# Optimization experiments

Measured on AMD Instinct MI355X. Metric: run time of the kernel, lower is better.

Reference implementation:

```python
import jax, jax.numpy as jnp
import numpy as np

D_MODEL = 512
D_AUX = 64
B, N = 8, 2048


def setup_inputs() -> dict:
    key = jax.random.key(0)
    ks = jax.random.split(key, 12)
    lim = 1.0 / np.sqrt(D_MODEL)  # torch Linear default init scale
    inp = {
        "x": jax.random.normal(ks[0], (B, N, D_MODEL), dtype=jnp.float32),
        "query_aux": jax.random.normal(ks[1], (B, N, D_AUX), dtype=jnp.float32),
        "key_aux": jax.random.normal(ks[2], (B, N, D_AUX), dtype=jnp.float32),
        "adjacency_mask": jax.random.randint(ks[3], (B, N, N), 0, 2, dtype=jnp.int32),
        "merge_coefficients": jnp.float32(0.3),
        "Wq": jax.random.uniform(ks[4], (D_MODEL, D_MODEL), jnp.float32, -lim, lim),
        "bq": jax.random.uniform(ks[5], (D_MODEL,), jnp.float32, -lim, lim),
        "Wk": jax.random.uniform(ks[6], (D_MODEL, D_MODEL), jnp.float32, -lim, lim),
        "bk": jax.random.uniform(ks[7], (D_MODEL,), jnp.float32, -lim, lim),
        "Wv": jax.random.uniform(ks[8], (D_MODEL, D_MODEL), jnp.float32, -lim, lim),
        "bv": jax.random.uniform(ks[9], (D_MODEL,), jnp.float32, -lim, lim),
        "threshold": jnp.float32(0.5),
    }
    return inp


def reference(x, query_aux, key_aux, adjacency_mask, merge_coefficients,
              Wq, bq, Wk, bk, Wv, bv, threshold):
    d_model = x.shape[-1]
    d_aux = key_aux.shape[-1]
    scale = jnp.asarray(d_model, x.dtype) ** 0.5
    scale_aux = jnp.asarray(d_aux, x.dtype) ** 0.5

    q = x @ Wq.T + bq  # [B,N,D]
    k = x @ Wk.T + bk
    v = x @ Wv.T + bv

    scores = jnp.einsum('bnd,bmd->bnm', q, k) / scale  # [B,N,N]
    scores_aux = jnp.einsum('bnd,bmd->bnm', query_aux, key_aux) / scale_aux

    # data-dependent merge: where aux score nonzero AND score above learned threshold
    merge_mask = (scores_aux != 0) & (scores > threshold)
    merged = (1.0 - merge_coefficients) * scores + merge_coefficients * scores_aux
    scores = jnp.where(merge_mask, merged, scores)

    mask_value = jnp.finfo(scores.dtype).min
    scores = jnp.where(adjacency_mask == 0, mask_value, scores)

    weights = jax.nn.softmax(scores, axis=-1)
    return jnp.einsum('bnm,bmd->bnd', weights, v)
```

## Files before the change

kernel.cpp:

```cpp
#include <hip/hip_runtime.h>
#include <cstdint>

#define SEQ    2048
#define DM     512
#define DAUX   64

typedef _Float16 f16;
typedef __attribute__((ext_vector_type(2))) _Float16 f16x2;
typedef __attribute__((ext_vector_type(4))) _Float16 f16x4;
typedef __attribute__((ext_vector_type(8))) _Float16 f16x8;
typedef __attribute__((ext_vector_type(4))) float fx4;
typedef __attribute__((ext_vector_type(16))) float fx16;

__device__ __forceinline__ void g2l16(const void* g, void* l) {
  __builtin_amdgcn_global_load_lds(
      (__attribute__((address_space(1))) void*)const_cast<void*>(g),
      (__attribute__((address_space(3))) void*)l, 16, 0, 0);
}

__device__ __forceinline__ void stage32(const f16* __restrict__ g0, int stride,
                                        f16* lds, int t) {
#pragma unroll
  for (int p = 0; p < 2; ++p) {
    int L = p * 256 + t;
    int row = L >> 2;
    int jp = L & 3;
    int jl = jp ^ ((row >> 1) & 3);
    g2l16(g0 + (size_t)row * stride + jl * 8, lds + L * 8);
  }
}
__device__ __forceinline__ f16x8 frag32(const f16* lds, int row, int kq) {
  int jp = (kq >> 3) ^ ((row >> 1) & 3);
  return *(const f16x8*)(lds + row * 32 + jp * 8);
}

__device__ __forceinline__ void stage64(const f16* __restrict__ g0, int stride,
                                        f16* lds, int t) {
#pragma unroll
  for (int p = 0; p < 4; ++p) {
    int L = p * 256 + t;
    int row = L >> 3;
    int jp = L & 7;
    int jl = jp ^ (row & 7);
    g2l16(g0 + (size_t)row * stride + jl * 8, lds + L * 8);
  }
}
__device__ __forceinline__ f16x8 frag64(const f16* lds, int row, int kq) {
  int jp = (kq >> 3) ^ (row & 7);
  return *(const f16x8*)(lds + row * 64 + jp * 8);
}

__device__ __forceinline__ void chunk3_32(const f16* Ah, const f16* Al,
                                          const f16* Bh, const f16* Bl,
                                          fx16 acc[2][2], int wm, int wn, int lane) {
  const int r31 = lane & 31;
  const int kq = (lane >> 5) * 8;
#pragma unroll
  for (int k0 = 0; k0 < 32; k0 += 16) {
    f16x8 ah[2], al[2];
#pragma unroll
    for (int it = 0; it < 2; ++it) {
      int row = wm * 64 + it * 32 + r31;
      ah[it] = frag32(Ah, row, k0 + kq);
      al[it] = frag32(Al, row, k0 + kq);
    }
#pragma unroll
    for (int jt = 0; jt < 2; ++jt) {
      int col = wn * 64 + jt * 32 + r31;
      f16x8 bh = frag32(Bh, col, k0 + kq);
      f16x8 bl = frag32(Bl, col, k0 + kq);
#pragma unroll
      for (int it = 0; it < 2; ++it) {
        acc[it][jt] = __builtin_amdgcn_mfma_f32_32x32x16_f16(ah[it], bh, acc[it][jt], 0, 0, 0);
        acc[it][jt] = __builtin_amdgcn_mfma_f32_32x32x16_f16(ah[it], bl, acc[it][jt], 0, 0, 0);
        acc[it][jt] = __builtin_amdgcn_mfma_f32_32x32x16_f16(al[it], bh, acc[it][jt], 0, 0, 0);
      }
    }
  }
}

__device__ __forceinline__ void chunk1_64(const f16* A, const f16* B,
                                          fx16 acc[2][2], int wm, int wn, int lane) {
  const int r31 = lane & 31;
  const int kq = (lane >> 5) * 8;
#pragma unroll
  for (int k0 = 0; k0 < 64; k0 += 16) {
    f16x8 a[2];
#pragma unroll
    for (int it = 0; it < 2; ++it)
      a[it] = frag64(A, wm * 64 + it * 32 + r31, k0 + kq);
#pragma unroll
    for (int jt = 0; jt < 2; ++jt) {
      f16x8 b = frag64(B, wn * 64 + jt * 32 + r31, k0 + kq);
#pragma unroll
      for (int it = 0; it < 2; ++it)
        acc[it][jt] = __builtin_amdgcn_mfma_f32_32x32x16_f16(a[it], b, acc[it][jt], 0, 0, 0);
    }
  }
}

__global__ __launch_bounds__(256) void convert_split(
    const float* __restrict__ x, const float* __restrict__ Wq,
    const float* __restrict__ Wk, const float* __restrict__ Wv,
    f16* __restrict__ xh, f16* __restrict__ xl,
    f16* __restrict__ Wh, f16* __restrict__ Wl) {
  int idx = blockIdx.x * 256 + threadIdx.x;
  const float* src; f16* dh; f16* dl; size_t off;
  if (idx < 2097152) { src = x; off = (size_t)idx; dh = xh; dl = xl; }
  else {
    int rr = idx - 2097152;
    int w = rr >> 16, o = rr & 65535;
    src = (w == 0) ? Wq : (w == 1) ? Wk : Wv;
    off = (size_t)o;
    dh = Wh + (size_t)w * 262144; dl = Wl + (size_t)w * 262144;
  }
  float4 v = ((const float4*)src)[off];
  float vv[4] = {v.x, v.y, v.z, v.w};
  f16x4 hv, lv;
#pragma unroll
  for (int i = 0; i < 4; ++i) {
    float s = vv[i] * 32.0f;
    f16 hi = (f16)s;
    hv[i] = hi;
    lv[i] = (f16)(s - (float)hi);
  }
  *(f16x4*)(dh + off * 4) = hv;
  *(f16x4*)(dl + off * 4) = lv;
}

__global__ __launch_bounds__(256) void qkv_mfma(
    const f16* __restrict__ xh, const f16* __restrict__ xl,
    const f16* __restrict__ Wh, const f16* __restrict__ Wl,
    const float* __restrict__ bq, const float* __restrict__ bk, const float* __restrict__ bv,
    f16* __restrict__ qh, f16* __restrict__ ql,
    f16* __restrict__ kh, f16* __restrict__ kl,
    f16* __restrict__ vt) {
  __shared__ __align__(16) f16 sm[32768];
  const int t = threadIdx.x;
  const int i0 = blockIdx.x * 128, j0 = blockIdx.y * 128, z = blockIdx.z;
  const f16* WhZ = Wh + (size_t)z * 262144;
  const f16* WlZ = Wl + (size_t)z * 262144;
  const int lane = t & 63, wave = t >> 6;
  const int wm = wave >> 1, wn = wave & 1;
  const int r31 = lane & 31, half = lane >> 5;
  fx16 acc[2][2] = {};
  const f16* xhB = xh + (size_t)i0 * DM;
  const f16* xlB = xl + (size_t)i0 * DM;
  const f16* WhB = WhZ + (size_t)j0 * DM;
  const f16* WlB = WlZ + (size_t)j0 * DM;
  if (z < 2) {
    stage32(xhB, DM, sm, t);
    stage32(xlB, DM, sm + 4096, t);
    stage32(WhB, DM, sm + 8192, t);
    stage32(WlB, DM, sm + 12288, t);
    __syncthreads();
    for (int c = 0; c < 16; ++c) {
      f16* cur = sm + (c & 1) * 16384;
      if (c < 15) {
        f16* nxt = sm + ((c + 1) & 1) * 16384;
        int d0 = (c + 1) * 32;
        stage32(xhB + d0, DM, nxt, t);
        stage32(xlB + d0, DM, nxt + 4096, t);
        stage32(WhB + d0, DM, nxt + 8192, t);
        stage32(WlB + d0, DM, nxt + 12288, t);
      }
      chunk3_32(cur, cur + 4096, cur + 8192, cur + 12288, acc, wm, wn, lane);
      if (c < 15) __syncthreads();
    }
  } else {
    stage64(xhB, DM, sm, t);
    stage64(WhB, DM, sm + 8192, t);
    __syncthreads();
    for (int c = 0; c < 8; ++c) {
      f16* cur = sm + (c & 1) * 16384;
      if (c < 7) {
        f16* nxt = sm + ((c + 1) & 1) * 16384;
        int d0 = (c + 1) * 64;
        stage64(xhB + d0, DM, nxt, t);
        stage64(WhB + d0, DM, nxt + 8192, t);
      }
      chunk1_64(cur, cur + 8192, acc, wm, wn, lane);
      if (c < 7) __syncthreads();
    }
  }
  const float* bias = (z == 0) ? bq : (z == 1) ? bk : bv;
  if (z < 2) {
    f16* oh = z ? kh : qh;  f16* ol = z ? kl : ql;
#pragma unroll
    for (int it = 0; it < 2; ++it)
#pragma unroll
      for (int jt = 0; jt < 2; ++jt) {
        int j = j0 + wn * 64 + jt * 32 + r31;
        float bj = bias[j];
#pragma unroll
        for (int r = 0; r < 16; ++r) {
          int ib = i0 + wm * 64 + it * 32 + (r & 3) + 8 * (r >> 2) + 4 * half;
          float val = acc[it][jt][r] * (1.0f / 1024.0f) + bj;
          float s = val * 32.0f;
          f16 hi = (f16)s;
          oh[(size_t)ib * DM + j] = hi;
          ol[(size_t)ib * DM + j] = (f16)(s - (float)hi);
        }
      }
  } else {
#pragma unroll
    for (int it = 0; it < 2; ++it)
#pragma unroll
      for (int jt = 0; jt < 2; ++jt) {
        int j = j0 + wn * 64 + jt * 32 + r31;
        float bj = bias[j];
#pragma unroll
        for (int q4 = 0; q4 < 4; ++q4) {
          int ib = i0 + wm * 64 + it * 32 + 8 * q4 + 4 * half;
          int bb = ib >> 11, nb = ib & 2047;
          f16x4 hv;
#pragma unroll
          for (int g = 0; g < 4; ++g)
            hv[g] = (f16)(acc[it][jt][q4 * 4 + g] * (1.0f / 1024.0f) + bj);
          *(f16x4*)(vt + ((size_t)(bb * DM + j)) * SEQ + nb) = hv;
        }
      }
  }
}

__global__ __launch_bounds__(256) void scores_mfma(
    const f16* __restrict__ qh, const f16* __restrict__ ql,
    const f16* __restrict__ kh, const f16* __restrict__ kl,
    const float* __restrict__ qa, const float* __restrict__ ka,
    const int* __restrict__ adj,
    const float* __restrict__ mc_p, const float* __restrict__ thr_p,
    f16* __restrict__ S16) {
  __shared__ __align__(16) f16 sm[32768];
  const int t = threadIdx.x;
  const int n0 = blockIdx.x * 128, m0 = blockIdx.y * 128, b = blockIdx.z;
  const int lane = t & 63, wave = t >> 6;
  const int wm = wave >> 1, wn = wave & 1;
  const int r31 = lane & 31, half = lane >> 5;
  const int kq = half * 8;

  const f16* qhB = qh + ((size_t)b * SEQ + n0) * DM;
  const f16* qlB = ql + ((size_t)b * SEQ + n0) * DM;
  const f16* khB = kh + ((size_t)b * SEQ + m0) * DM;
  const f16* klB = kl + ((size_t)b * SEQ + m0) * DM;

  stage32(qhB, DM, sm, t);
  stage32(qlB, DM, sm + 4096, t);
  stage32(khB, DM, sm + 8192, t);
  stage32(klB, DM, sm + 12288, t);

  f16* QAl = sm + 16384;
  f16* KAl = sm + 24576;
  const float* QAb = qa + ((size_t)b * SEQ + n0) * DAUX;
  const float* KAb = ka + ((size_t)b * SEQ + m0) * DAUX;
#pragma unroll
  for (int p = 0; p < 4; ++p) {
    int L8 = p * 256 + t;
    int row = L8 >> 3, jb = L8 & 7;
    int c8 = jb * 8;
    int jp = jb ^ (row & 7);
    float4 u0 = *(const float4*)(QAb + (size_t)row * DAUX + c8);
    float4 u1 = *(const float4*)(QAb + (size_t)row * DAUX + c8 + 4);
    f16x8 hq = {(f16)u0.x,(f16)u0.y,(f16)u0.z,(f16)u0.w,(f16)u1.x,(f16)u1.y,(f16)u1.z,(f16)u1.w};
    *(f16x8*)(QAl + row * 64 + jp * 8) = hq;
    float4 w0 = *(const float4*)(KAb + (size_t)row * DAUX + c8);
    float4 w1 = *(const float4*)(KAb + (size_t)row * DAUX + c8 + 4);
    f16x8 hk = {(f16)w0.x,(f16)w0.y,(f16)w0.z,(f16)w0.w,(f16)w1.x,(f16)w1.y,(f16)w1.z,(f16)w1.w};
    *(f16x8*)(KAl + row * 64 + jp * 8) = hk;
  }
  __syncthreads();

  f16x2 sax2[2][2][8];
  {
    fx16 aacc[2][2] = {};
#pragma unroll
    for (int k0 = 0; k0 < 64; k0 += 16) {
      f16x8 qaf[2];
#pragma unroll
      for (int it = 0; it < 2; ++it)
        qaf[it] = frag64(QAl, wm * 64 + it * 32 + r31, k0 + kq);
#pragma unroll
      for (int jt = 0; jt < 2; ++jt) {
        f16x8 kaf = frag64(KAl, wn * 64 + jt * 32 + r31, k0 + kq);
#pragma unroll
        for (int it = 0; it < 2; ++it)
          aacc[it][jt] = __builtin_amdgcn_mfma_f32_32x32x16_f16(qaf[it], kaf, aacc[it][jt], 0, 0, 0);
      }
    }
#pragma unroll
    for (int it = 0; it < 2; ++it)
#pragma unroll
      for (int jt = 0; jt < 2; ++jt)
#pragma unroll
        for (int r = 0; r < 16; ++r)
          sax2[it][jt][r >> 1][r & 1] = (f16)aacc[it][jt][r];
  }
  __syncthreads();

  fx16 acc[2][2] = {};
  for (int c = 0; c < 16; ++c) {
    f16* cur = sm + (c & 1) * 16384;
    if (c < 15) {
      f16* nxt = sm + ((c + 1) & 1) * 16384;
      int d0 = (c + 1) * 32;
      stage32(qhB + d0, DM, nxt, t);
      stage32(qlB + d0, DM, nxt + 4096, t);
      stage32(khB + d0, DM, nxt + 8192, t);
      stage32(klB + d0, DM, nxt + 12288, t);
    }
    chunk3_32(cur, cur + 4096, cur + 8192, cur + 12288, acc, wm, wn, lane);
    if (c < 15) __syncthreads();
  }

  const float mc = *mc_p, thr = *thr_p;
  const float invC = 1.0f / (1024.0f * 22.62741699796952f);
#pragma unroll
  for (int it = 0; it < 2; ++it)
#pragma unroll
    for (int jt = 0; jt < 2; ++jt) {
      int col = m0 + wn * 64 + jt * 32 + r31;
#pragma unroll
      for (int r = 0; r < 16; ++r) {
        int row = n0 + wm * 64 + it * 32 + (r & 3) + 8 * (r >> 2) + 4 * half;
        size_t rbase = ((size_t)b * SEQ + row) * SEQ;
        float s = acc[it][jt][r] * invC;
        float sa = (float)sax2[it][jt][r >> 1][r & 1] * 0.125f;
        if (sa != 0.0f && s > thr) s = (1.0f - mc) * s + mc * sa;
        if (adj[rbase + col] == 0) s = -65504.0f;
        S16[rbase + col] = (f16)s;
      }
    }
}

__global__ __launch_bounds__(256) void softmax_p(
    f16* __restrict__ S16, float* __restrict__ rowsum) {
  const int wv = threadIdx.x >> 6, ln = threadIdx.x & 63;
  const size_t row = (size_t)blockIdx.x * 4 + wv;
  f16* Sr = S16 + row * SEQ;
  f16x8 v[4];
  float vals[32];
#pragma unroll
  for (int j = 0; j < 4; ++j) {
    v[j] = *(const f16x8*)(Sr + j * 512 + ln * 8);
#pragma unroll
    for (int i = 0; i < 8; ++i) vals[j * 8 + i] = (float)v[j][i];
  }
  float m = vals[0];
#pragma unroll
  for (int i = 1; i < 32; ++i) m = fmaxf(m, vals[i]);
#pragma unroll
  for (int off = 1; off < 64; off <<= 1) m = fmaxf(m, __shfl_xor(m, off, 64));
  float z = 0.f;
  f16x8 p16[4];
#pragma unroll
  for (int j = 0; j < 4; ++j)
#pragma unroll
    for (int i = 0; i < 8; ++i) {
      f16 p = (f16)(__expf(vals[j * 8 + i] - m) * 1024.0f);
      p16[j][i] = p;
      z += (float)p;
    }
#pragma unroll
  for (int off = 1; off < 64; off <<= 1) z += __shfl_xor(z, off, 64);
  if (ln == 0) rowsum[row] = z;
#pragma unroll
  for (int j = 0; j < 4; ++j)
    *(f16x8*)(Sr + j * 512 + ln * 8) = p16[j];
}

__global__ __launch_bounds__(256) void pv_mfma(
    const f16* __restrict__ P16, const f16* __restrict__ vt,
    const float* __restrict__ rowsum, float* __restrict__ O) {
  __shared__ __align__(16) f16 sm[32768];
  const int t = threadIdx.x;
  const int n0 = blockIdx.x * 128, d0 = blockIdx.y * 128, b = blockIdx.z;
  const int lane = t & 63, wave = t >> 6;
  const int wm = wave >> 1, wn = wave & 1;
  const int r31 = lane & 31, half = lane >> 5;
  fx16 acc[2][2] = {};
  const f16* Pb = P16 + ((size_t)b * SEQ + n0) * SEQ;
  const f16* Vb = vt + ((size_t)b * DM + d0) * SEQ;
  stage64(Pb, SEQ, sm, t);
  stage64(Vb, SEQ, sm + 8192, t);
  __syncthreads();
  for (int c = 0; c < 32; ++c) {
    f16* cur = sm + (c & 1) * 16384;
    if (c < 31) {
      f16* nxt = sm + ((c + 1) & 1) * 16384;
      int m0 = (c + 1) * 64;
      stage64(Pb + m0, SEQ, nxt, t);
      stage64(Vb + m0, SEQ, nxt + 8192, t);
    }
    chunk1_64(cur, cur + 8192, acc, wm, wn, lane);
    if (c < 31) __syncthreads();
  }
#pragma unroll
  for (int it = 0; it < 2; ++it)
#pragma unroll
    for (int jt = 0; jt < 2; ++jt) {
      int d = d0 + wn * 64 + jt * 32 + r31;
#pragma unroll
      for (int r = 0; r < 16; ++r) {
        int n = n0 + wm * 64 + it * 32 + (r & 3) + 8 * (r >> 2) + 4 * half;
        float inv = 1.0f / rowsum[(size_t)b * SEQ + n];
        O[((size_t)b * SEQ + n) * DM + d] = acc[it][jt][r] * inv;
      }
    }
}

extern "C" void kernel_launch(void* const* d_in, const int* in_sizes, int n_in,
                              void* d_out, int out_size, void* d_ws, size_t ws_size,
                              hipStream_t stream) {
  const float* x   = (const float*)d_in[0];
  const float* qa  = (const float*)d_in[1];
  const float* ka  = (const float*)d_in[2];
  const int*   adj = (const int*)d_in[3];
  const float* mc  = (const float*)d_in[4];
  const float* Wq  = (const float*)d_in[5];
  const float* bq  = (const float*)d_in[6];
  const float* Wk  = (const float*)d_in[7];
  const float* bk  = (const float*)d_in[8];
  const float* Wv  = (const float*)d_in[9];
  const float* bv  = (const float*)d_in[10];
  const float* thr = (const float*)d_in[11];
  float* out = (float*)d_out;

  f16* qh  = (f16*)d_ws;
  f16* ql  = qh + 8388608;
  f16* kh  = ql + 8388608;
  f16* kl  = kh + 8388608;
  f16* vt  = kl + 8388608;
  f16* S16 = vt + 8388608;
  float* rowsum = (float*)(S16 + 33554432);
  f16* xh = S16;
  f16* xl = xh + 8388608;
  f16* Wh = xl + 8388608;
  f16* Wl = Wh + 786432;

  convert_split<<<8960, 256, 0, stream>>>(x, Wq, Wk, Wv, xh, xl, Wh, Wl);
  qkv_mfma<<<dim3(128, 4, 3), 256, 0, stream>>>(xh, xl, Wh, Wl, bq, bk, bv,
                                                qh, ql, kh, kl, vt);
  scores_mfma<<<dim3(16, 16, 8), 256, 0, stream>>>(qh, ql, kh, kl, qa, ka, adj,
                                                   mc, thr, S16);
  softmax_p<<<4096, 256, 0, stream>>>(S16, rowsum);
  pv_mfma<<<dim3(16, 4, 8), 256, 0, stream>>>(S16, vt, rowsum, out);
}
```

Baseline: 502.4 us.

## Single-buffer LDS tiles, interleave hi/lo halves, raise occupancy to three blocks

Replaces the double-buffered 64 KB LDS pipelines in the QKV, scores and PV GEMM kernels with a single 32 KB buffer, synchronized before and after each stage. The hi and lo f16 halves now share one 64-wide swizzled row. Launch bounds request three blocks per CU to hide memory latency through occupancy instead of software prefetch. The scores kernel also computes the aux scores after the main loop and keeps them in fp32 registers, which drops the f16 repacking. The cost is an extra barrier per iteration and no overlap of load and compute within a block.

```diff
diff --git a/kernel.cpp b/kernel.cpp
--- a/kernel.cpp
+++ b/kernel.cpp
@@ -18,20 +18,22 @@
       (__attribute__((address_space(3))) void*)l, 16, 0, 0);
 }
 
-__device__ __forceinline__ void stage32(const f16* __restrict__ g0, int stride,
-                                        f16* lds, int t) {
-#pragma unroll
-  for (int p = 0; p < 2; ++p) {
+__device__ __forceinline__ void stagec(const f16* __restrict__ hi,
+                                       const f16* __restrict__ lo,
+                                       int stride, f16* lds, int t) {
+#pragma unroll
+  for (int p = 0; p < 4; ++p) {
     int L = p * 256 + t;
-    int row = L >> 2;
-    int jp = L & 3;
-    int jl = jp ^ ((row >> 1) & 3);
-    g2l16(g0 + (size_t)row * stride + jl * 8, lds + L * 8);
-  }
-}
-__device__ __forceinline__ f16x8 frag32(const f16* lds, int row, int kq) {
-  int jp = (kq >> 3) ^ ((row >> 1) & 3);
-  return *(const f16x8*)(lds + row * 32 + jp * 8);
+    int row = L >> 3, jb = L & 7;
+    int jl = jb ^ (row & 7);
+    const f16* src = (jl < 4) ? hi + (size_t)row * stride + jl * 8
+                              : lo + (size_t)row * stride + (jl - 4) * 8;
+    g2l16(src, lds + L * 8);
+  }
+}
+__device__ __forceinline__ f16x8 fragc(const f16* lds, int row, int jl) {
+  int jp = jl ^ (row & 7);
+  return *(const f16x8*)(lds + row * 64 + jp * 8);
 }
 
 __device__ __forceinline__ void stage64(const f16* __restrict__ g0, int stride,
@@ -39,9 +41,8 @@
 #pragma unroll
   for (int p = 0; p < 4; ++p) {
     int L = p * 256 + t;
-    int row = L >> 3;
-    int jp = L & 7;
-    int jl = jp ^ (row & 7);
+    int row = L >> 3, jb = L & 7;
+    int jl = jb ^ (row & 7);
     g2l16(g0 + (size_t)row * stride + jl * 8, lds + L * 8);
   }
 }
@@ -50,25 +51,25 @@
   return *(const f16x8*)(lds + row * 64 + jp * 8);
 }
 
-__device__ __forceinline__ void chunk3_32(const f16* Ah, const f16* Al,
-                                          const f16* Bh, const f16* Bl,
-                                          fx16 acc[2][2], int wm, int wn, int lane) {
+__device__ __forceinline__ void chunk3c(const f16* A, const f16* B,
+                                        fx16 acc[2][2], int wm, int wn, int lane) {
   const int r31 = lane & 31;
-  const int kq = (lane >> 5) * 8;
+  const int half8 = (lane >> 5) * 8;
 #pragma unroll
   for (int k0 = 0; k0 < 32; k0 += 16) {
+    int kb = (k0 + half8) >> 3;
     f16x8 ah[2], al[2];
 #pragma unroll
     for (int it = 0; it < 2; ++it) {
       int row = wm * 64 + it * 32 + r31;
-      ah[it] = frag32(Ah, row, k0 + kq);
-      al[it] = frag32(Al, row, k0 + kq);
+      ah[it] = fragc(A, row, kb);
+      al[it] = fragc(A, row, kb + 4);
     }
 #pragma unroll
     for (int jt = 0; jt < 2; ++jt) {
       int col = wn * 64 + jt * 32 + r31;
-      f16x8 bh = frag32(Bh, col, k0 + kq);
-      f16x8 bl = frag32(Bl, col, k0 + kq);
+      f16x8 bh = fragc(B, col, kb);
+      f16x8 bl = fragc(B, col, kb + 4);
 #pragma unroll
       for (int it = 0; it < 2; ++it) {
         acc[it][jt] = __builtin_amdgcn_mfma_f32_32x32x16_f16(ah[it], bh, acc[it][jt], 0, 0, 0);
@@ -128,14 +129,14 @@
   *(f16x4*)(dl + off * 4) = lv;
 }
 
-__global__ __launch_bounds__(256) void qkv_mfma(
+__global__ __launch_bounds__(256, 3) void qkv_mfma(
     const f16* __restrict__ xh, const f16* __restrict__ xl,
     const f16* __restrict__ Wh, const f16* __restrict__ Wl,
     const float* __restrict__ bq, const float* __restrict__ bk, const float* __restrict__ bv,
     f16* __restrict__ qh, f16* __restrict__ ql,
     f16* __restrict__ kh, f16* __restrict__ kl,
     f16* __restrict__ vt) {
-  __shared__ __align__(16) f16 sm[32768];
+  __shared__ __align__(16) f16 sm[16384];
   const int t = threadIdx.x;
   const int i0 = blockIdx.x * 128, j0 = blockIdx.y * 128, z = blockIdx.z;
   const f16* WhZ = Wh + (size_t)z * 262144;
@@ -149,38 +150,22 @@
   const f16* WhB = WhZ + (size_t)j0 * DM;
   const f16* WlB = WlZ + (size_t)j0 * DM;
   if (z < 2) {
-    stage32(xhB, DM, sm, t);
-    stage32(xlB, DM, sm + 4096, t);
-    stage32(WhB, DM, sm + 8192, t);
-    stage32(WlB, DM, sm + 12288, t);
-    __syncthreads();
     for (int c = 0; c < 16; ++c) {
-      f16* cur = sm + (c & 1) * 16384;
-      if (c < 15) {
-        f16* nxt = sm + ((c + 1) & 1) * 16384;
-        int d0 = (c + 1) * 32;
-        stage32(xhB + d0, DM, nxt, t);
-        stage32(xlB + d0, DM, nxt + 4096, t);
-        stage32(WhB + d0, DM, nxt + 8192, t);
-        stage32(WlB + d0, DM, nxt + 12288, t);
-      }
-      chunk3_32(cur, cur + 4096, cur + 8192, cur + 12288, acc, wm, wn, lane);
-      if (c < 15) __syncthreads();
+      int d0 = c * 32;
+      __syncthreads();
+      stagec(xhB + d0, xlB + d0, DM, sm, t);
+      stagec(WhB + d0, WlB + d0, DM, sm + 8192, t);
+      __syncthreads();
+      chunk3c(sm, sm + 8192, acc, wm, wn, lane);
     }
   } else {
-    stage64(xhB, DM, sm, t);
-    stage64(WhB, DM, sm + 8192, t);
-    __syncthreads();
     for (int c = 0; c < 8; ++c) {
-      f16* cur = sm + (c & 1) * 16384;
-      if (c < 7) {
-        f16* nxt = sm + ((c + 1) & 1) * 16384;
-        int d0 = (c + 1) * 64;
-        stage64(xhB + d0, DM, nxt, t);
-        stage64(WhB + d0, DM, nxt + 8192, t);
-      }
-      chunk1_64(cur, cur + 8192, acc, wm, wn, lane);
-      if (c < 7) __syncthreads();
+      int d0 = c * 64;
+      __syncthreads();
+      stage64(xhB + d0, DM, sm, t);
+      stage64(WhB + d0, DM, sm + 8192, t);
+      __syncthreads();
+      chunk1_64(sm, sm + 8192, acc, wm, wn, lane);
     }
   }
   const float* bias = (z == 0) ? bq : (z == 1) ? bk : bv;
@@ -223,14 +208,14 @@
   }
 }
 
-__global__ __launch_bounds__(256) void scores_mfma(
+__global__ __launch_bounds__(256, 3) void scores_mfma(
     const f16* __restrict__ qh, const f16* __restrict__ ql,
     const f16* __restrict__ kh, const f16* __restrict__ kl,
     const float* __restrict__ qa, const float* __restrict__ ka,
     const int* __restrict__ adj,
     const float* __restrict__ mc_p, const float* __restrict__ thr_p,
     f16* __restrict__ S16) {
-  __shared__ __align__(16) f16 sm[32768];
+  __shared__ __align__(16) f16 sm[16384];
   const int t = threadIdx.x;
   const int n0 = blockIdx.x * 128, m0 = blockIdx.y * 128, b = blockIdx.z;
   const int lane = t & 63, wave = t >> 6;
@@ -243,13 +228,19 @@
   const f16* khB = kh + ((size_t)b * SEQ + m0) * DM;
   const f16* klB = kl + ((size_t)b * SEQ + m0) * DM;
 
-  stage32(qhB, DM, sm, t);
-  stage32(qlB, DM, sm + 4096, t);
-  stage32(khB, DM, sm + 8192, t);
-  stage32(klB, DM, sm + 12288, t);
-
-  f16* QAl = sm + 16384;
-  f16* KAl = sm + 24576;
+  fx16 acc[2][2] = {};
+  for (int c = 0; c < 16; ++c) {
+    int d0 = c * 32;
+    __syncthreads();
+    stagec(qhB + d0, qlB + d0, DM, sm, t);
+    stagec(khB + d0, klB + d0, DM, sm + 8192, t);
+    __syncthreads();
+    chunk3c(sm, sm + 8192, acc, wm, wn, lane);
+  }
+
+  __syncthreads();
+  f16* QAl = sm;
+  f16* KAl = sm + 8192;
   const float* QAb = qa + ((size_t)b * SEQ + n0) * DAUX;
   const float* KAb = ka + ((size_t)b * SEQ + m0) * DAUX;
 #pragma unroll
@@ -268,47 +259,20 @@
     *(f16x8*)(KAl + row * 64 + jp * 8) = hk;
   }
   __syncthreads();
-
-  f16x2 sax2[2][2][8];
-  {
-    fx16 aacc[2][2] = {};
-#pragma unroll
-    for (int k0 = 0; k0 < 64; k0 += 16) {
-      f16x8 qaf[2];
+  fx16 aacc[2][2] = {};
+#pragma unroll
+  for (int k0 = 0; k0 < 64; k0 += 16) {
+    f16x8 qaf[2];
+#pragma unroll
+    for (int it = 0; it < 2; ++it)
+      qaf[it] = frag64(QAl, wm * 64 + it * 32 + r31, k0 + kq);
+#pragma unroll
+    for (int jt = 0; jt < 2; ++jt) {
+      f16x8 kaf = frag64(KAl, wn * 64 + jt * 32 + r31, k0 + kq);
 #pragma unroll
       for (int it = 0; it < 2; ++it)
-        qaf[it] = frag64(QAl, wm * 64 + it * 32 + r31, k0 + kq);
-#pragma unroll
-      for (int jt = 0; jt < 2; ++jt) {
-        f16x8 kaf = frag64(KAl, wn * 64 + jt * 32 + r31, k0 + kq);
-#pragma unroll
-        for (int it = 0; it < 2; ++it)
-          aacc[it][jt] = __builtin_amdgcn_mfma_f32_32x32x16_f16(qaf[it], kaf, aacc[it][jt], 0, 0, 0);
-      }
-    }
-#pragma unroll
-    for (int it = 0; it < 2; ++it)
-#pragma unroll
-      for (int jt = 0; jt < 2; ++jt)
-#pragma unroll
-        for (int r = 0; r < 16; ++r)
-          sax2[it][jt][r >> 1][r & 1] = (f16)aacc[it][jt][r];
-  }
-  __syncthreads();
-
-  fx16 acc[2][2] = {};
-  for (int c = 0; c < 16; ++c) {
-    f16* cur = sm + (c & 1) * 16384;
-    if (c < 15) {
-      f16* nxt = sm + ((c + 1) & 1) * 16384;
-      int d0 = (c + 1) * 32;
-      stage32(qhB + d0, DM, nxt, t);
-      stage32(qlB + d0, DM, nxt + 4096, t);
-      stage32(khB + d0, DM, nxt + 8192, t);
-      stage32(klB + d0, DM, nxt + 12288, t);
-    }
-    chunk3_32(cur, cur + 4096, cur + 8192, cur + 12288, acc, wm, wn, lane);
-    if (c < 15) __syncthreads();
+        aacc[it][jt] = __builtin_amdgcn_mfma_f32_32x32x16_f16(qaf[it], kaf, aacc[it][jt], 0, 0, 0);
+    }
   }
 
   const float mc = *mc_p, thr = *thr_p;
@@ -323,7 +287,7 @@
         int row = n0 + wm * 64 + it * 32 + (r & 3) + 8 * (r >> 2) + 4 * half;
         size_t rbase = ((size_t)b * SEQ + row) * SEQ;
         float s = acc[it][jt][r] * invC;
-        float sa = (float)sax2[it][jt][r >> 1][r & 1] * 0.125f;
+        float sa = aacc[it][jt][r] * 0.125f;
         if (sa != 0.0f && s > thr) s = (1.0f - mc) * s + mc * sa;
         if (adj[rbase + col] == 0) s = -65504.0f;
         S16[rbase + col] = (f16)s;
@@ -367,10 +331,10 @@
     *(f16x8*)(Sr + j * 512 + ln * 8) = p16[j];
 }
 
-__global__ __launch_bounds__(256) void pv_mfma(
+__global__ __launch_bounds__(256, 3) void pv_mfma(
     const f16* __restrict__ P16, const f16* __restrict__ vt,
     const float* __restrict__ rowsum, float* __restrict__ O) {
-  __shared__ __align__(16) f16 sm[32768];
+  __shared__ __align__(16) f16 sm[16384];
   const int t = threadIdx.x;
   const int n0 = blockIdx.x * 128, d0 = blockIdx.y * 128, b = blockIdx.z;
   const int lane = t & 63, wave = t >> 6;
@@ -379,19 +343,13 @@
   fx16 acc[2][2] = {};
   const f16* Pb = P16 + ((size_t)b * SEQ + n0) * SEQ;
   const f16* Vb = vt + ((size_t)b * DM + d0) * SEQ;
-  stage64(Pb, SEQ, sm, t);
-  stage64(Vb, SEQ, sm + 8192, t);
-  __syncthreads();
   for (int c = 0; c < 32; ++c) {
-    f16* cur = sm + (c & 1) * 16384;
-    if (c < 31) {
-      f16* nxt = sm + ((c + 1) & 1) * 16384;
-      int m0 = (c + 1) * 64;
-      stage64(Pb + m0, SEQ, nxt, t);
-      stage64(Vb + m0, SEQ, nxt + 8192, t);
-    }
-    chunk1_64(cur, cur + 8192, acc, wm, wn, lane);
-    if (c < 31) __syncthreads();
+    int m0 = c * 64;
+    __syncthreads();
+    stage64(Pb + m0, SEQ, sm, t);
+    stage64(Vb + m0, SEQ, sm + 8192, t);
+    __syncthreads();
+    chunk1_64(sm, sm + 8192, acc, wm, wn, lane);
   }
 #pragma unroll
   for (int it = 0; it < 2; ++it)
```

Result: slower. 557.1 us (+10.9%).
